# Kernel tuning notes

Measured on AMD Instinct MI355X. Metric: run time of the kernel, lower is better.

The kernel has to match this reference:

```python
import jax, jax.numpy as jnp
import numpy as np

B, S, E, H = 2, 2048, 1024, 16
D = E // H  # head dim = 64
ROPE_BASE = 10000.0


def _rope(x):
    # x: [B, H, S, D]; interleaved-pair rotary embeddings (torchtune style)
    d2 = D // 2
    theta = 1.0 / (ROPE_BASE ** (jnp.arange(d2, dtype=jnp.float32) * 2.0 / D))  # [D/2]
    pos = jnp.arange(S, dtype=jnp.float32)
    ang = pos[:, None] * theta[None, :]            # [S, D/2]
    cos, sin = jnp.cos(ang), jnp.sin(ang)          # broadcast over B,H
    xr = x.reshape(B, H, S, d2, 2)
    x1, x2 = xr[..., 0], xr[..., 1]
    o1 = x1 * cos - x2 * sin
    o2 = x1 * sin + x2 * cos
    return jnp.stack([o1, o2], axis=-1).reshape(B, H, S, D)


def setup_inputs() -> dict:
    key = jax.random.key(0)
    ks = jax.random.split(key, 5)
    scale = 1.0 / np.sqrt(E)
    return {
        "x": jax.random.normal(ks[0], (B, S, E), dtype=jnp.float32),
        "Wq": jax.random.normal(ks[1], (E, E), dtype=jnp.float32) * scale,
        "Wk": jax.random.normal(ks[2], (E, E), dtype=jnp.float32) * scale,
        "Wv": jax.random.normal(ks[3], (E, E), dtype=jnp.float32) * scale,
        "Wo": jax.random.normal(ks[4], (E, E), dtype=jnp.float32) * scale,
    }


def reference(x, Wq, Wk, Wv, Wo):
    # torch Linear: y = x @ W^T
    def proj(W):
        return (x @ W.T).reshape(B, S, H, D).transpose(0, 2, 1, 3)  # [B,H,S,D]

    q = _rope(proj(Wq))
    k = _rope(proj(Wk))
    v = proj(Wv)

    attn_scale = 1.0 / np.sqrt(E)  # faithful: scales by sqrt(d_embed), not head dim
    scores = jnp.einsum('bhqd,bhkd->bhqk', q, k) * attn_scale  # [B,H,S,S]
    causal = jnp.tril(jnp.ones((S, S), dtype=bool))
    scores = jnp.where(causal, scores, -jnp.inf)
    probs = jax.nn.softmax(scores, axis=-1)
    out = jnp.einsum('bhqk,bhkd->bhqd', probs, v)  # [B,H,S,D]
    out = out.transpose(0, 2, 1, 3).reshape(B, S, E)
    return out @ Wo.T
```

## Files before the change

kernel.cpp:

```cpp
#include <hip/hip_runtime.h>
#include <hip/hip_bf16.h>
#include <math.h>

typedef __bf16 bf16;
typedef __bf16 bf16x8 __attribute__((ext_vector_type(8)));
typedef float f32x4 __attribute__((ext_vector_type(4)));

#define SEQ 2048
#define EMB 1024
#define NH  16
#define HD  64
#define NROWS 4096

#define GLOAD_LDS16(gp, lp)                                             \
    __builtin_amdgcn_global_load_lds(                                   \
        (const __attribute__((address_space(1))) void*)(gp),            \
        (__attribute__((address_space(3))) void*)(lp), 16, 0, 0)

#define QSCALE 0.045084439f

__global__ __launch_bounds__(256) void cvt_rope_kernel(
    const float* __restrict__ x,  const float* __restrict__ Wq,
    const float* __restrict__ Wk, const float* __restrict__ Wv,
    const float* __restrict__ Wo,
    bf16* __restrict__ xb, bf16* __restrict__ Wqb, bf16* __restrict__ Wkb,
    bf16* __restrict__ Wvb, bf16* __restrict__ Wob,
    float* __restrict__ ctab, float* __restrict__ stab)
{
    int b = blockIdx.x;
    if (b >= 4096) {
        int t = (b - 4096) * 256 + threadIdx.x;
        int s = t >> 5;
        int j = t & 31;
        double freq = pow(10000.0, -(double)j / 32.0);
        double ang = (double)s * freq;
        ctab[t] = (float)cos(ang);
        stab[t] = (float)sin(ang);
        return;
    }
    const float* src; bf16* dst; int boff;
    if      (b < 2048) { src = x;  dst = xb;  boff = b;        }
    else if (b < 2560) { src = Wq; dst = Wqb; boff = b - 2048; }
    else if (b < 3072) { src = Wk; dst = Wkb; boff = b - 2560; }
    else if (b < 3584) { src = Wv; dst = Wvb; boff = b - 3072; }
    else               { src = Wo; dst = Wob; boff = b - 3584; }
    size_t off = (size_t)boff * 2048 + (size_t)threadIdx.x * 8;
    float4 f0 = *(const float4*)(src + off);
    float4 f1 = *(const float4*)(src + off + 4);
    bf16x8 v;
    v[0] = (bf16)f0.x; v[1] = (bf16)f0.y; v[2] = (bf16)f0.z; v[3] = (bf16)f0.w;
    v[4] = (bf16)f1.x; v[5] = (bf16)f1.y; v[6] = (bf16)f1.z; v[7] = (bf16)f1.w;
    *(bf16x8*)(dst + off) = v;
}

__global__ __launch_bounds__(256) void qkv_rope_kernel(
    const bf16* __restrict__ x,
    const bf16* __restrict__ Wq, const bf16* __restrict__ Wk, const bf16* __restrict__ Wv,
    const float* __restrict__ ctab, const float* __restrict__ stab,
    bf16* __restrict__ qf_ws, bf16* __restrict__ kf_ws, bf16* __restrict__ vf_ws)
{
    __shared__ __align__(16) bf16 SMEM[16384];
    bf16* As = SMEM;
    bf16* Bs = SMEM + 4096;

    const int t    = threadIdx.x;
    const int lane = t & 63;
    const int wave = t >> 6;
    const int col  = lane & 15;
    const int quad = lane >> 4;

    const int nblk = blockIdx.x;
    const int m0   = blockIdx.y * 128;

    const bf16* W; int nloc;
    if (nblk < 8)       { W = Wq; nloc = nblk * 128; }
    else if (nblk < 16) { W = Wk; nloc = (nblk - 8) * 128; }
    else                { W = Wv; nloc = (nblk - 16) * 128; }

    const bf16 *ga[2], *gb[2];
#pragma unroll
    for (int j = 0; j < 2; j++) {
        int c = t + j * 256;
        ga[j] = x + (size_t)(m0 + (c >> 2)) * EMB + (c & 3) * 8;
        gb[j] = W + (size_t)(nloc + (c >> 2)) * EMB + (c & 3) * 8;
    }

    const int wm = (wave >> 1) * 64;
    const int wn = (wave & 1) * 64;

    f32x4 acc[4][4];
#pragma unroll
    for (int i = 0; i < 4; i++)
#pragma unroll
        for (int j = 0; j < 4; j++) acc[i][j] = (f32x4){0.f, 0.f, 0.f, 0.f};

    for (int kc = 0; kc < EMB; kc += 32) {
#pragma unroll
        for (int j = 0; j < 2; j++) {
            int c = t + j * 256;
            GLOAD_LDS16(ga[j] + kc, As + c * 8);
            GLOAD_LDS16(gb[j] + kc, Bs + c * 8);
        }
        __syncthreads();
        bf16x8 a[4], b[4];
#pragma unroll
        for (int mt = 0; mt < 4; mt++)
            a[mt] = *(const bf16x8*)(As + (wm + mt * 16 + col) * 32 + quad * 8);
#pragma unroll
        for (int nt = 0; nt < 4; nt++)
            b[nt] = *(const bf16x8*)(Bs + (wn + nt * 16 + col) * 32 + quad * 8);
#pragma unroll
        for (int mt = 0; mt < 4; mt++)
#pragma unroll
            for (int nt = 0; nt < 4; nt++)
                acc[mt][nt] = __builtin_amdgcn_mfma_f32_16x16x32_bf16(a[mt], b[nt], acc[mt][nt], 0, 0, 0);
        __syncthreads();
    }

    bf16* Es = SMEM + wave * 4096;

    const int n0w  = nblk * 128 + wn;
    const int m0w  = m0 + wm;
    const int bb_  = m0w >> 11;
    const int ss0  = m0w & (SEQ - 1);
    const int h    = (n0w >> 6) & 15;
    const int bh   = bb_ * NH + h;
    const int kind = (n0w < 1024) ? 0 : (n0w < 2048 ? 1 : 2);

#pragma unroll
    for (int mt = 0; mt < 4; mt++) {
#pragma unroll
        for (int nt = 0; nt < 4; nt++) {
            const int d  = nt * 16 + col;
            const int jj = d >> 1;
#pragma unroll
            for (int r = 0; r < 4; r++) {
                const int ss_l = mt * 16 + quad * 4 + r;
                float v = acc[mt][nt][r];
                if (kind < 2) {
                    float partner = __shfl_xor(v, 1, 64);
                    float c  = ctab[(ss0 + ss_l) * 32 + jj];
                    float sn = stab[(ss0 + ss_l) * 32 + jj];
                    float o = ((d & 1) == 0) ? (v * c - partner * sn)
                                             : (partner * sn + v * c);
                    if (kind == 0) o *= QSCALE;
                    int eoff = ((ss_l >> 4) * 2 + (d >> 5)) * 512
                             + ((d >> 3) & 3) * 128 + (ss_l & 15) * 8 + (d & 7);
                    Es[eoff] = (bf16)o;
                } else {
                    int eoff = ((ss_l >> 5) * 4 + (d >> 4)) * 512
                             + ((ss_l >> 3) & 3) * 128 + (d & 15) * 8 + (ss_l & 7);
                    Es[eoff] = (bf16)v;
                }
            }
        }
    }

    bf16* base;
    if (kind == 0)      base = qf_ws + ((size_t)bh * 128 + (ss0 >> 4)) * 1024;
    else if (kind == 1) base = kf_ws + ((size_t)bh * 128 + (ss0 >> 4)) * 1024;
    else                base = vf_ws + ((size_t)bh * 64 + (ss0 >> 5)) * 2048;
#pragma unroll
    for (int i = 0; i < 8; i++) {
        bf16x8 vv = *(const bf16x8*)&Es[i * 512 + lane * 8];
        *(bf16x8*)(base + i * 512 + lane * 8) = vv;
    }
}

__global__ __launch_bounds__(128) void attn_kernel(
    const bf16* __restrict__ qf, const bf16* __restrict__ kf,
    const bf16* __restrict__ vf, bf16* __restrict__ attn_ws)
{
    __shared__ float comb_o[2][4][4][64];
    __shared__ float comb_l[2][64];

    const int lane = threadIdx.x & 63;
    const int wave = threadIdx.x >> 6;
    const int col  = lane & 15;
    const int quad = lane >> 4;

    const int qt = 63 - (int)(blockIdx.x >> 5);
    const int bh = blockIdx.x & 31;
    const int b_ = bh >> 4;
    const int h  = bh & 15;
    const int qb = qt * 32;
    const int nk = qt + 1;

    const bf16* Qf = qf + (size_t)bh * 131072;
    const bf16* Kf = kf + (size_t)bh * 131072;
    const bf16* Vf = vf + (size_t)bh * 131072;

    bf16x8 aq[2][2];
#pragma unroll
    for (int f = 0; f < 2; f++) {
        const bf16* qp = Qf + (size_t)(qt * 2 + f) * 1024 + lane * 8;
        aq[f][0] = *(const bf16x8*)(qp);
        aq[f][1] = *(const bf16x8*)(qp + 512);
    }

    f32x4 acc_o[2][4];
#pragma unroll
    for (int f = 0; f < 2; f++)
#pragma unroll
        for (int i = 0; i < 4; i++) acc_o[f][i] = (f32x4){0.f, 0.f, 0.f, 0.f};
    float lsum[2] = {0.f, 0.f};

    int psrc[8];
#pragma unroll
    for (int j = 0; j < 8; j++)
        psrc[j] = ((((quad * 2 + (j >> 2)) & 3) << 4) | col) << 2;

    int s0 = (wave < nk) ? wave : 0;
    bf16x8 Ka[2][2], nKa[2][2];
    {
        const bf16* p = Kf + (size_t)s0 * 2048 + lane * 8;
        Ka[0][0] = *(const bf16x8*)(p);
        Ka[0][1] = *(const bf16x8*)(p + 512);
        Ka[1][0] = *(const bf16x8*)(p + 1024);
        Ka[1][1] = *(const bf16x8*)(p + 1536);
    }

    for (int s = wave; s < nk; s += 2) {
        bf16x8 Vb[4];
        {
            const bf16* p = Vf + (size_t)s * 2048 + lane * 8;
            Vb[0] = *(const bf16x8*)(p);
            Vb[1] = *(const bf16x8*)(p + 512);
            Vb[2] = *(const bf16x8*)(p + 1024);
            Vb[3] = *(const bf16x8*)(p + 1536);
        }

        f32x4 sT[2][2];
#pragma unroll
        for (int g = 0; g < 2; g++)
#pragma unroll
            for (int f = 0; f < 2; f++) {
                f32x4 z = (f32x4){0.f, 0.f, 0.f, 0.f};
                z = __builtin_amdgcn_mfma_f32_16x16x32_bf16(Ka[g][0], aq[f][0], z, 0, 0, 0);
                z = __builtin_amdgcn_mfma_f32_16x16x32_bf16(Ka[g][1], aq[f][1], z, 0, 0, 0);
                sT[g][f] = z;
            }

        {
            int sn = (s + 2 < nk) ? s + 2 : s;
            const bf16* p = Kf + (size_t)sn * 2048 + lane * 8;
            nKa[0][0] = *(const bf16x8*)(p);
            nKa[0][1] = *(const bf16x8*)(p + 512);
            nKa[1][0] = *(const bf16x8*)(p + 1024);
            nKa[1][1] = *(const bf16x8*)(p + 1536);
        }

        float p[2][2][4];
        if (s == nk - 1) {
#pragma unroll
            for (int g = 0; g < 2; g++)
#pragma unroll
                for (int f = 0; f < 2; f++) {
                    const int qg = qb + f * 16 + col;
#pragma unroll
                    for (int r = 0; r < 4; r++) {
                        int key = s * 32 + g * 16 + quad * 4 + r;
                        float e = (key <= qg) ? exp2f(sT[g][f][r]) : 0.f;
                        p[g][f][r] = e;
                        lsum[f] += e;
                    }
                }
        } else {
#pragma unroll
            for (int g = 0; g < 2; g++)
#pragma unroll
                for (int f = 0; f < 2; f++)
#pragma unroll
                    for (int r = 0; r < 4; r++) {
                        float e = exp2f(sT[g][f][r]);
                        p[g][f][r] = e;
                        lsum[f] += e;
                    }
        }

#pragma unroll
        for (int f = 0; f < 2; f++) {
            unsigned int pk[4];
#pragma unroll
            for (int r = 0; r < 4; r++) {
                unsigned int lo = __builtin_bit_cast(unsigned short, (bf16)p[0][f][r]);
                unsigned int hi = __builtin_bit_cast(unsigned short, (bf16)p[1][f][r]);
                pk[r] = (hi << 16) | lo;
            }
            bf16x8 a_p;
#pragma unroll
            for (int j = 0; j < 8; j++) {
                unsigned int g = (unsigned int)__builtin_amdgcn_ds_bpermute(psrc[j], (int)pk[j & 3]);
                unsigned short bits = (quad < 2) ? (unsigned short)(g & 0xffff)
                                                 : (unsigned short)(g >> 16);
                a_p[j] = __builtin_bit_cast(bf16, bits);
            }
#pragma unroll
            for (int nt = 0; nt < 4; nt++)
                acc_o[f][nt] = __builtin_amdgcn_mfma_f32_16x16x32_bf16(a_p, Vb[nt], acc_o[f][nt], 0, 0, 0);
        }

        Ka[0][0] = nKa[0][0]; Ka[0][1] = nKa[0][1];
        Ka[1][0] = nKa[1][0]; Ka[1][1] = nKa[1][1];
    }

    if (wave == 1) {
#pragma unroll
        for (int f = 0; f < 2; f++) {
            comb_l[f][lane] = lsum[f];
#pragma unroll
            for (int nt = 0; nt < 4; nt++)
#pragma unroll
                for (int r = 0; r < 4; r++)
                    comb_o[f][nt][r][lane] = acc_o[f][nt][r];
        }
    }
    __syncthreads();

    if (wave == 0) {
#pragma unroll
        for (int f = 0; f < 2; f++) {
            lsum[f] += comb_l[f][lane];
#pragma unroll
            for (int nt = 0; nt < 4; nt++)
#pragma unroll
                for (int r = 0; r < 4; r++)
                    acc_o[f][nt][r] += comb_o[f][nt][r][lane];
        }

#pragma unroll
        for (int f = 0; f < 2; f++) {
            lsum[f] += __shfl_xor(lsum[f], 16, 64);
            lsum[f] += __shfl_xor(lsum[f], 32, 64);
        }
#pragma unroll
        for (int f = 0; f < 2; f++)
#pragma unroll
            for (int r = 0; r < 4; r++) {
                float l_r = __shfl(lsum[f], quad * 4 + r, 64);
                float inv = 1.0f / l_r;
                int q = qb + f * 16 + quad * 4 + r;
                bf16* orow = attn_ws + (size_t)(b_ * SEQ + q) * EMB + h * HD;
#pragma unroll
                for (int nt = 0; nt < 4; nt++)
                    orow[nt * 16 + col] = (bf16)(acc_o[f][nt][r] * inv);
            }
    }
}

__global__ __launch_bounds__(256) void oproj_kernel(
    const bf16* __restrict__ attn_ws, const bf16* __restrict__ Wo,
    float* __restrict__ out)
{
    __shared__ __align__(16) char SM[36864];
    bf16* As = (bf16*)SM;
    bf16* Bs = (bf16*)(SM + 8192);

    const int t    = threadIdx.x;
    const int lane = t & 63;
    const int wave = t >> 6;
    const int col  = lane & 15;
    const int quad = lane >> 4;

    const int n0 = blockIdx.x * 64;
    const int m0 = blockIdx.y * 128;

    const bf16 *ga[2], *gb;
#pragma unroll
    for (int j = 0; j < 2; j++) {
        int c = t + j * 256;
        ga[j] = attn_ws + (size_t)(m0 + (c >> 2)) * EMB + (c & 3) * 8;
    }
    gb = Wo + (size_t)(n0 + (t >> 2)) * EMB + (t & 3) * 8;

    const int wm = (wave >> 1) * 64;
    const int wn = (wave & 1) * 32;

    f32x4 acc[4][2];
#pragma unroll
    for (int i = 0; i < 4; i++)
#pragma unroll
        for (int j = 0; j < 2; j++) acc[i][j] = (f32x4){0.f, 0.f, 0.f, 0.f};

    for (int kc = 0; kc < EMB; kc += 32) {
#pragma unroll
        for (int j = 0; j < 2; j++) {
            int c = t + j * 256;
            GLOAD_LDS16(ga[j] + kc, As + c * 8);
        }
        GLOAD_LDS16(gb + kc, Bs + t * 8);
        __syncthreads();
        bf16x8 a[4], b[2];
#pragma unroll
        for (int mt = 0; mt < 4; mt++)
            a[mt] = *(const bf16x8*)(As + (wm + mt * 16 + col) * 32 + quad * 8);
#pragma unroll
        for (int nt = 0; nt < 2; nt++)
            b[nt] = *(const bf16x8*)(Bs + (wn + nt * 16 + col) * 32 + quad * 8);
#pragma unroll
        for (int mt = 0; mt < 4; mt++)
#pragma unroll
            for (int nt = 0; nt < 2; nt++)
                acc[mt][nt] = __builtin_amdgcn_mfma_f32_16x16x32_bf16(a[mt], b[nt], acc[mt][nt], 0, 0, 0);
        __syncthreads();
    }

    float* Os = (float*)(SM + (size_t)wave * 9216);
#pragma unroll
    for (int mt = 0; mt < 4; mt++)
#pragma unroll
        for (int nt = 0; nt < 2; nt++)
#pragma unroll
            for (int r = 0; r < 4; r++)
                Os[(mt * 16 + quad * 4 + r) * 36 + nt * 16 + col] = acc[mt][nt][r];

    const int row = lane >> 3, c8 = lane & 7;
    float* obase = out + (size_t)(m0 + wm) * EMB + n0 + wn;
#pragma unroll
    for (int i = 0; i < 8; i++) {
        float4 vv = *(const float4*)&Os[(i * 8 + row) * 36 + c8 * 4];
        *(float4*)(obase + (size_t)(i * 8 + row) * EMB + c8 * 4) = vv;
    }
}

extern "C" void kernel_launch(void* const* d_in, const int* in_sizes, int n_in,
                              void* d_out, int out_size, void* d_ws, size_t ws_size,
                              hipStream_t stream) {
    const float* x  = (const float*)d_in[0];
    const float* Wq = (const float*)d_in[1];
    const float* Wk = (const float*)d_in[2];
    const float* Wv = (const float*)d_in[3];
    const float* Wo = (const float*)d_in[4];
    float* out = (float*)d_out;

    char* ws = (char*)d_ws;
    bf16* qf_ws   = (bf16*)(ws);
    bf16* kf_ws   = (bf16*)(ws + (8u  << 20));
    bf16* vf_ws   = (bf16*)(ws + (16u << 20));
    bf16* xb      = (bf16*)(ws + (24u << 20));
    bf16* attn_ws = (bf16*)(ws + (24u << 20));
    bf16* Wqb     = (bf16*)(ws + (32u << 20));
    bf16* Wkb     = (bf16*)(ws + (34u << 20));
    bf16* Wvb     = (bf16*)(ws + (36u << 20));
    bf16* Wob     = (bf16*)(ws + (38u << 20));
    float* ctab   = (float*)(ws + (40u << 20));
    float* stab   = ctab + SEQ * 32;

    hipLaunchKernelGGL(cvt_rope_kernel, dim3(4352), dim3(256), 0, stream,
                       x, Wq, Wk, Wv, Wo, xb, Wqb, Wkb, Wvb, Wob, ctab, stab);
    hipLaunchKernelGGL(qkv_rope_kernel, dim3(24, 32), dim3(256), 0, stream,
                       xb, Wqb, Wkb, Wvb, ctab, stab, qf_ws, kf_ws, vf_ws);
    hipLaunchKernelGGL(attn_kernel, dim3(2048), dim3(128), 0, stream,
                       qf_ws, kf_ws, vf_ws, attn_ws);
    hipLaunchKernelGGL(oproj_kernel, dim3(16, 32), dim3(256), 0, stream,
                       attn_ws, Wob, out);
}
```

Before: 185.4 us.

## Share K/V tiles across waves via double-buffered LDS with 64-row query blocks

Each block now handles 64 query rows, two waves of 32 rows each, instead of splitting the key range of 32 rows between two waves. K and V tiles are streamed into double-buffered shared memory with global_load_lds, so both waves reuse one fetch. This replaces per-wave register prefetch from global memory and removes the cross-wave partial-sum combine. In exchange the grid is halved to 1024 blocks, each iteration adds a block-wide barrier, and the causal workload per block is less balanced.

```diff
diff --git a/kernel.cpp b/kernel.cpp
--- a/kernel.cpp
+++ b/kernel.cpp
@@ -171,20 +171,22 @@
     const bf16* __restrict__ qf, const bf16* __restrict__ kf,
     const bf16* __restrict__ vf, bf16* __restrict__ attn_ws)
 {
-    __shared__ float comb_o[2][4][4][64];
-    __shared__ float comb_l[2][64];
-
-    const int lane = threadIdx.x & 63;
-    const int wave = threadIdx.x >> 6;
+    __shared__ __align__(16) bf16 Kt[2][2048];
+    __shared__ __align__(16) bf16 Vt[2][2048];
+
+    const int t    = threadIdx.x;
+    const int lane = t & 63;
+    const int wave = t >> 6;
     const int col  = lane & 15;
     const int quad = lane >> 4;
 
-    const int qt = 63 - (int)(blockIdx.x >> 5);
+    const int qt = 31 - (int)(blockIdx.x >> 5);
     const int bh = blockIdx.x & 31;
     const int b_ = bh >> 4;
     const int h  = bh & 15;
-    const int qb = qt * 32;
-    const int nk = qt + 1;
+    const int qb = qt * 64;
+    const int qw = qb + wave * 32;
+    const int nk = 2 * qt + 2;
 
     const bf16* Qf = qf + (size_t)bh * 131072;
     const bf16* Kf = kf + (size_t)bh * 131072;
@@ -193,7 +195,7 @@
     bf16x8 aq[2][2];
 #pragma unroll
     for (int f = 0; f < 2; f++) {
-        const bf16* qp = Qf + (size_t)(qt * 2 + f) * 1024 + lane * 8;
+        const bf16* qp = Qf + (size_t)(qt * 4 + wave * 2 + f) * 1024 + lane * 8;
         aq[f][0] = *(const bf16x8*)(qp);
         aq[f][1] = *(const bf16x8*)(qp + 512);
     }
@@ -210,25 +212,38 @@
     for (int j = 0; j < 8; j++)
         psrc[j] = ((((quad * 2 + (j >> 2)) & 3) << 4) | col) << 2;
 
-    int s0 = (wave < nk) ? wave : 0;
-    bf16x8 Ka[2][2], nKa[2][2];
-    {
-        const bf16* p = Kf + (size_t)s0 * 2048 + lane * 8;
-        Ka[0][0] = *(const bf16x8*)(p);
-        Ka[0][1] = *(const bf16x8*)(p + 512);
-        Ka[1][0] = *(const bf16x8*)(p + 1024);
-        Ka[1][1] = *(const bf16x8*)(p + 1536);
-    }
-
-    for (int s = wave; s < nk; s += 2) {
-        bf16x8 Vb[4];
-        {
-            const bf16* p = Vf + (size_t)s * 2048 + lane * 8;
-            Vb[0] = *(const bf16x8*)(p);
-            Vb[1] = *(const bf16x8*)(p + 512);
-            Vb[2] = *(const bf16x8*)(p + 1024);
-            Vb[3] = *(const bf16x8*)(p + 1536);
-        }
+#pragma unroll
+    for (int j = 0; j < 2; j++) {
+        int c = (t + j * 128) * 8;
+        GLOAD_LDS16(Kf + c, &Kt[0][c]);
+        GLOAD_LDS16(Vf + c, &Vt[0][c]);
+    }
+    __syncthreads();
+
+    for (int s = 0; s < nk; s++) {
+        const int cur = s & 1;
+
+        if (s + 1 < nk) {
+            const int nb = cur ^ 1;
+            const bf16* ks = Kf + (size_t)(s + 1) * 2048;
+            const bf16* vs = Vf + (size_t)(s + 1) * 2048;
+#pragma unroll
+            for (int j = 0; j < 2; j++) {
+                int c = (t + j * 128) * 8;
+                GLOAD_LDS16(ks + c, &Kt[nb][c]);
+                GLOAD_LDS16(vs + c, &Vt[nb][c]);
+            }
+        }
+
+        bf16x8 Ka[2][2], Vb[4];
+#pragma unroll
+        for (int g = 0; g < 2; g++) {
+            Ka[g][0] = *(const bf16x8*)&Kt[cur][g * 1024 + lane * 8];
+            Ka[g][1] = *(const bf16x8*)&Kt[cur][g * 1024 + 512 + lane * 8];
+        }
+#pragma unroll
+        for (int nt = 0; nt < 4; nt++)
+            Vb[nt] = *(const bf16x8*)&Vt[cur][nt * 512 + lane * 8];
 
         f32x4 sT[2][2];
 #pragma unroll
@@ -241,22 +256,13 @@
                 sT[g][f] = z;
             }
 
-        {
-            int sn = (s + 2 < nk) ? s + 2 : s;
-            const bf16* p = Kf + (size_t)sn * 2048 + lane * 8;
-            nKa[0][0] = *(const bf16x8*)(p);
-            nKa[0][1] = *(const bf16x8*)(p + 512);
-            nKa[1][0] = *(const bf16x8*)(p + 1024);
-            nKa[1][1] = *(const bf16x8*)(p + 1536);
-        }
-
         float p[2][2][4];
-        if (s == nk - 1) {
+        if (s >= nk - 2) {
 #pragma unroll
             for (int g = 0; g < 2; g++)
 #pragma unroll
                 for (int f = 0; f < 2; f++) {
-                    const int qg = qb + f * 16 + col;
+                    const int qg = qw + f * 16 + col;
 #pragma unroll
                     for (int r = 0; r < 4; r++) {
                         int key = s * 32 + g * 16 + quad * 4 + r;
@@ -300,52 +306,26 @@
                 acc_o[f][nt] = __builtin_amdgcn_mfma_f32_16x16x32_bf16(a_p, Vb[nt], acc_o[f][nt], 0, 0, 0);
         }
 
-        Ka[0][0] = nKa[0][0]; Ka[0][1] = nKa[0][1];
-        Ka[1][0] = nKa[1][0]; Ka[1][1] = nKa[1][1];
-    }
-
-    if (wave == 1) {
-#pragma unroll
-        for (int f = 0; f < 2; f++) {
-            comb_l[f][lane] = lsum[f];
+        __syncthreads();
+    }
+
+#pragma unroll
+    for (int f = 0; f < 2; f++) {
+        lsum[f] += __shfl_xor(lsum[f], 16, 64);
+        lsum[f] += __shfl_xor(lsum[f], 32, 64);
+    }
+#pragma unroll
+    for (int f = 0; f < 2; f++)
+#pragma unroll
+        for (int r = 0; r < 4; r++) {
+            float l_r = __shfl(lsum[f], quad * 4 + r, 64);
+            float inv = 1.0f / l_r;
+            int q = qw + f * 16 + quad * 4 + r;
+            bf16* orow = attn_ws + (size_t)(b_ * SEQ + q) * EMB + h * HD;
 #pragma unroll
             for (int nt = 0; nt < 4; nt++)
-#pragma unroll
-                for (int r = 0; r < 4; r++)
-                    comb_o[f][nt][r][lane] = acc_o[f][nt][r];
-        }
-    }
-    __syncthreads();
-
-    if (wave == 0) {
-#pragma unroll
-        for (int f = 0; f < 2; f++) {
-            lsum[f] += comb_l[f][lane];
-#pragma unroll
-            for (int nt = 0; nt < 4; nt++)
-#pragma unroll
-                for (int r = 0; r < 4; r++)
-                    acc_o[f][nt][r] += comb_o[f][nt][r][lane];
-        }
-
-#pragma unroll
-        for (int f = 0; f < 2; f++) {
-            lsum[f] += __shfl_xor(lsum[f], 16, 64);
-            lsum[f] += __shfl_xor(lsum[f], 32, 64);
-        }
-#pragma unroll
-        for (int f = 0; f < 2; f++)
-#pragma unroll
-            for (int r = 0; r < 4; r++) {
-                float l_r = __shfl(lsum[f], quad * 4 + r, 64);
-                float inv = 1.0f / l_r;
-                int q = qb + f * 16 + quad * 4 + r;
-                bf16* orow = attn_ws + (size_t)(b_ * SEQ + q) * EMB + h * HD;
-#pragma unroll
-                for (int nt = 0; nt < 4; nt++)
-                    orow[nt * 16 + col] = (bf16)(acc_o[f][nt][r] * inv);
-            }
-    }
+                orow[nt * 16 + col] = (bf16)(acc_o[f][nt][r] * inv);
+        }
 }
 
 __global__ __launch_bounds__(256) void oproj_kernel(
@@ -450,7 +430,7 @@
                        x, Wq, Wk, Wv, Wo, xb, Wqb, Wkb, Wvb, Wob, ctab, stab);
     hipLaunchKernelGGL(qkv_rope_kernel, dim3(24, 32), dim3(256), 0, stream,
                        xb, Wqb, Wkb, Wvb, ctab, stab, qf_ws, kf_ws, vf_ws);
-    hipLaunchKernelGGL(attn_kernel, dim3(2048), dim3(128), 0, stream,
+    hipLaunchKernelGGL(attn_kernel, dim3(1024), dim3(128), 0, stream,
                        qf_ws, kf_ws, vf_ws, attn_ws);
     hipLaunchKernelGGL(oproj_kernel, dim3(16, 32), dim3(256), 0, stream,
                        attn_ws, Wob, out);
```

After: 216.5 us. +16.8%, slower.
